# Performance work log

Hardware: AMD Instinct MI355X
Metric: run time of the kernel (lower is better)

Reference implementation:

```python
import jax, jax.numpy as jnp
import numpy as np


def setup_inputs() -> dict:
    key = jax.random.key(0)
    k1, k2 = jax.random.split(key)
    surfaces = jax.random.normal(k1, (4, 4096, 3), dtype=jnp.float32)   # [S, N, K]
    targets = jax.random.normal(k2, (16384, 3), dtype=jnp.float32)      # [M, K]
    return {"surfaces": surfaces, "targets": targets}


def reference(surfaces, targets):
    # Pairwise squared distances ||a-b||^2 = ||a||^2 + ||b||^2 - 2 a.b
    # surfaces: [S, N, K], targets: [M, K]
    a2 = jnp.sum(surfaces * surfaces, axis=-1)          # [S, N]
    b2 = jnp.sum(targets * targets, axis=-1)            # [M]
    ab = jnp.einsum('snk,mk->snm', surfaces, targets)   # [S, N, M]
    dist = a2[:, :, None] + b2[None, None, :] - 2.0 * ab  # [S, N, M]
    # direction='cloud2nearest' -> dim=0: min over surface points N per target
    nearest = jnp.min(dist, axis=1)                     # [S, M]
    # stack over surfaces then min over dim 0 (S)
    nearest = jnp.min(nearest, axis=0)                  # [M]
    return jnp.sum(nearest)
```

## Files before the change

### kernel.cpp

```cpp
#include <hip/hip_runtime.h>
#include <cfloat>


namespace {
constexpr int M   = 16384;
constexpr int SN  = 16384;
constexpr int TPB = 256;
constexpr int T   = 8;
constexpr int TGT_PER_BLOCK = TPB * T;
constexpr int NCHUNK = 128;
constexpr int CHUNK  = SN / NCHUNK;
constexpr int K2B    = 256;
}

__global__ __launch_bounds__(TPB, 4) void dist_partial_min(
    const float* __restrict__ surf,
    const float* __restrict__ tgt,
    float* __restrict__ wmin,
    unsigned* __restrict__ counter)
{
  __shared__ alignas(16) float4 spt[CHUNK];

  const int tid   = threadIdx.x;
  const int mbase = blockIdx.x * TGT_PER_BLOCK;
  const int cbase = blockIdx.y * CHUNK;

  if (blockIdx.x == 0 && blockIdx.y == 0 && tid == 0) counter[0] = 0u;

  if (tid < CHUNK) {
    const float* s = surf + (size_t)(cbase + tid) * 3;
    const float x = s[0], y = s[1], z = s[2];
    spt[tid] = make_float4(x, y, z, fmaf(x, x, fmaf(y, y, z * z)));
  }

  float tx[T], ty[T], tz[T], b2[T], mn[T];
#pragma unroll
  for (int j = 0; j < T; ++j) {
    const int m     = mbase + j * TPB + tid;
    const float* tp = tgt + (size_t)m * 3;
    const float a = tp[0], b = tp[1], c = tp[2];
    tx[j] = -2.0f * a; ty[j] = -2.0f * b; tz[j] = -2.0f * c;
    b2[j] = fmaf(a, a, fmaf(b, b, c * c));
    mn[j] = FLT_MAX;
  }
  __syncthreads();

  float4 C0 = spt[0], C1 = spt[1], C2 = spt[2], C3 = spt[3];
  for (int p = 0; p < CHUNK; p += 4) {
    const int pn = (p + 4) & (CHUNK - 1);
    const float4 N0 = spt[pn + 0];
    const float4 N1 = spt[pn + 1];
    const float4 N2 = spt[pn + 2];
    const float4 N3 = spt[pn + 3];
#pragma unroll
    for (int j = 0; j < T; ++j) {
      const float d0 = fmaf(C0.x, tx[j], fmaf(C0.y, ty[j], fmaf(C0.z, tz[j], C0.w)));
      const float d1 = fmaf(C1.x, tx[j], fmaf(C1.y, ty[j], fmaf(C1.z, tz[j], C1.w)));
      const float d2 = fmaf(C2.x, tx[j], fmaf(C2.y, ty[j], fmaf(C2.z, tz[j], C2.w)));
      const float d3 = fmaf(C3.x, tx[j], fmaf(C3.y, ty[j], fmaf(C3.z, tz[j], C3.w)));
      mn[j] = fminf(fminf(mn[j], d0), d1);
      mn[j] = fminf(fminf(mn[j], d2), d3);
    }
    C0 = N0; C1 = N1; C2 = N2; C3 = N3;
  }

#pragma unroll
  for (int j = 0; j < T; ++j)
    wmin[(size_t)blockIdx.y * M + mbase + j * TPB + tid] = mn[j] + b2[j];
}

__global__ __launch_bounds__(256) void dist_min_sum(
    const float* __restrict__ wmin,
    float* __restrict__ part,
    unsigned* __restrict__ counter,
    float* __restrict__ out)
{
  const int tid  = threadIdx.x;
  const int lane = tid & 63;
  const int w    = tid >> 6;
  const int m    = blockIdx.x * 64 + lane;

  float mnv = FLT_MAX;
  const int c0 = w * (NCHUNK / 4);
#pragma unroll 8
  for (int c = 0; c < NCHUNK / 4; ++c)
    mnv = fminf(mnv, wmin[(size_t)(c0 + c) * M + m]);

  __shared__ float red[4][64];
  red[w][lane] = mnv;
  __syncthreads();

  if (w == 0) {
    float v = fminf(fminf(red[0][lane], red[1][lane]),
                    fminf(red[2][lane], red[3][lane]));
    for (int off = 32; off; off >>= 1) v += __shfl_down(v, off, 64);

    unsigned done = 0;
    if (lane == 0) {
      part[blockIdx.x] = v;
      __threadfence();
      done = atomicAdd(counter, 1u);
    }
    done = __shfl(done, 0, 64);

    if (done == (unsigned)(K2B - 1)) {
      __threadfence();
      float s = 0.0f;
#pragma unroll
      for (int i = 0; i < K2B / 64; ++i) s += part[i * 64 + lane];
      for (int off = 32; off; off >>= 1) s += __shfl_down(s, off, 64);
      if (lane == 0) out[0] = s;
    }
  }
}

extern "C" void kernel_launch(void* const* d_in, const int* in_sizes, int n_in,
                              void* d_out, int out_size, void* d_ws, size_t ws_size,
                              hipStream_t stream) {
  const float* surf = (const float*)d_in[0];
  const float* tgt  = (const float*)d_in[1];
  float* out = (float*)d_out;

  float*    wmin    = (float*)d_ws;
  float*    part    = wmin + (size_t)NCHUNK * M;
  unsigned* counter = (unsigned*)(part + K2B);

  dim3 g1(M / TGT_PER_BLOCK, NCHUNK);
  dist_partial_min<<<g1, TPB, 0, stream>>>(surf, tgt, wmin, counter);
  dist_min_sum<<<K2B, 256, 0, stream>>>(wmin, part, counter, out);
}
```

Measured before the change: 40.34 us.

## Compute pairwise distances with bf16 split-precision MFMA instead of scalar FMA

Adds a prep kernel that encodes surface points and targets as hi/lo bf16 split rows, padded to K=32, so that one 16x16x32 MFMA produces a² − 2a·b with roughly fp32 accuracy. The main kernel streams surface rows from global memory into the matrix cores and reduces each output tile with fminf. It uses 32 chunks instead of 128, which shrinks the partial-min buffer, and b² is now added in the final reduction. This trades VALU FMA work for matrix-core throughput at the cost of an extra launch, zero-padded K, and some loss of precision from the bf16 splitting.

```diff
diff --git a/kernel.cpp b/kernel.cpp
--- a/kernel.cpp
+++ b/kernel.cpp
@@ -5,72 +5,133 @@
 namespace {
 constexpr int M   = 16384;
 constexpr int SN  = 16384;
-constexpr int TPB = 256;
-constexpr int T   = 8;
-constexpr int TGT_PER_BLOCK = TPB * T;
-constexpr int NCHUNK = 128;
-constexpr int CHUNK  = SN / NCHUNK;
-constexpr int K2B    = 256;
+constexpr int NCH = 32;
+constexpr int PPC = SN / NCH;
+constexpr int NG  = 128;
+constexpr int TPG = 128;
+constexpr int K2B = 256;
 }
 
-__global__ __launch_bounds__(TPB, 4) void dist_partial_min(
-    const float* __restrict__ surf,
-    const float* __restrict__ tgt,
-    float* __restrict__ wmin,
-    unsigned* __restrict__ counter)
+typedef short bf16x8 __attribute__((ext_vector_type(8)));
+typedef float f32x4  __attribute__((ext_vector_type(4)));
+
+static __device__ __forceinline__ unsigned short f2bf(float f) {
+  unsigned int u = __builtin_bit_cast(unsigned int, f);
+  return (unsigned short)((u + 0x7FFFu + ((u >> 16) & 1u)) >> 16);
+}
+static __device__ __forceinline__ float bf2f(unsigned short h) {
+  unsigned int u = ((unsigned int)h) << 16;
+  return __builtin_bit_cast(float, u);
+}
+
+__global__ __launch_bounds__(256) void build_ab(
+    const float* __restrict__ surf, const float* __restrict__ tgt,
+    unsigned short* __restrict__ Aex, unsigned short* __restrict__ Bex,
+    float* __restrict__ b2f, unsigned* __restrict__ counter)
 {
-  __shared__ alignas(16) float4 spt[CHUNK];
+  const int i = blockIdx.x * 256 + threadIdx.x;
+  if (i == 0) counter[0] = 0u;
 
-  const int tid   = threadIdx.x;
-  const int mbase = blockIdx.x * TGT_PER_BLOCK;
-  const int cbase = blockIdx.y * CHUNK;
+  {
+    const float x = surf[(size_t)i*3+0], y = surf[(size_t)i*3+1], z = surf[(size_t)i*3+2];
+    const float s2 = fmaf(x, x, fmaf(y, y, z * z));
+    unsigned short row[32];
+#pragma unroll
+    for (int k = 0; k < 32; ++k) row[k] = 0;
+    const float cs[3] = {x, y, z};
+#pragma unroll
+    for (int c = 0; c < 3; ++c) {
+      const unsigned short hi = f2bf(cs[c]);
+      const unsigned short lo = f2bf(cs[c] - bf2f(hi));
+      row[3*c+0] = hi; row[3*c+1] = hi; row[3*c+2] = lo;
+    }
+    const unsigned short shi = f2bf(s2);
+    const unsigned short slo = f2bf(s2 - bf2f(shi));
+    row[9] = shi; row[10] = slo;
+#pragma unroll
+    for (int k = 0; k < 16; ++k)
+      ((unsigned int*)(Aex + (size_t)i*32))[k] =
+          (unsigned int)row[2*k] | ((unsigned int)row[2*k+1] << 16);
+  }
+  {
+    const float a = tgt[(size_t)i*3+0], b = tgt[(size_t)i*3+1], c = tgt[(size_t)i*3+2];
+    b2f[i] = fmaf(a, a, fmaf(b, b, c * c));
+    const float us[3] = {-2.0f*a, -2.0f*b, -2.0f*c};
+    unsigned short row[32];
+#pragma unroll
+    for (int k = 0; k < 32; ++k) row[k] = 0;
+#pragma unroll
+    for (int q = 0; q < 3; ++q) {
+      const unsigned short hi = f2bf(us[q]);
+      const unsigned short lo = f2bf(us[q] - bf2f(hi));
+      row[3*q+0] = hi; row[3*q+1] = lo; row[3*q+2] = hi;
+    }
+    const unsigned short one = f2bf(1.0f);
+    row[9] = one; row[10] = one;
+#pragma unroll
+    for (int k = 0; k < 16; ++k)
+      ((unsigned int*)(Bex + (size_t)i*32))[k] =
+          (unsigned int)row[2*k] | ((unsigned int)row[2*k+1] << 16);
+  }
+}
 
-  if (blockIdx.x == 0 && blockIdx.y == 0 && tid == 0) counter[0] = 0u;
+__global__ __launch_bounds__(256, 4) void dist_mfma(
+    const unsigned short* __restrict__ Aex,
+    const unsigned short* __restrict__ Bex,
+    float* __restrict__ wmin)
+{
+  const int tid  = threadIdx.x;
+  const int lane = tid & 63;
+  const int wid  = tid >> 6;
+  const int wg   = blockIdx.x * 4 + wid;
+  const int g    = wg & (NG - 1);
+  const int c    = wg >> 7;
+  const int m0   = g * TPG;
+  const int r15  = lane & 15;
+  const int koff = (lane >> 4) * 8;
 
-  if (tid < CHUNK) {
-    const float* s = surf + (size_t)(cbase + tid) * 3;
-    const float x = s[0], y = s[1], z = s[2];
-    spt[tid] = make_float4(x, y, z, fmaf(x, x, fmaf(y, y, z * z)));
-  }
+  bf16x8 bfr[8];
+#pragma unroll
+  for (int f = 0; f < 8; ++f)
+    bfr[f] = *(const bf16x8*)(Bex + ((size_t)(m0 + f*16 + r15)) * 32 + koff);
 
-  float tx[T], ty[T], tz[T], b2[T], mn[T];
+  float mn[8];
 #pragma unroll
-  for (int j = 0; j < T; ++j) {
-    const int m     = mbase + j * TPB + tid;
-    const float* tp = tgt + (size_t)m * 3;
-    const float a = tp[0], b = tp[1], c = tp[2];
-    tx[j] = -2.0f * a; ty[j] = -2.0f * b; tz[j] = -2.0f * c;
-    b2[j] = fmaf(a, a, fmaf(b, b, c * c));
-    mn[j] = FLT_MAX;
-  }
-  __syncthreads();
+  for (int f = 0; f < 8; ++f) mn[f] = FLT_MAX;
 
-  float4 C0 = spt[0], C1 = spt[1], C2 = spt[2], C3 = spt[3];
-  for (int p = 0; p < CHUNK; p += 4) {
-    const int pn = (p + 4) & (CHUNK - 1);
-    const float4 N0 = spt[pn + 0];
-    const float4 N1 = spt[pn + 1];
-    const float4 N2 = spt[pn + 2];
-    const float4 N3 = spt[pn + 3];
+  const int pbase = c * PPC;
+  const unsigned short* ap = Aex + ((size_t)(pbase + r15)) * 32 + koff;
+
+  bf16x8 acur = *(const bf16x8*)ap;
+  for (int r = 0; r < PPC / 16; ++r) {
+    const int rn = (r + 1 < PPC / 16) ? r + 1 : r;
+    const bf16x8 anxt = *(const bf16x8*)(ap + (size_t)rn * 16 * 32);
 #pragma unroll
-    for (int j = 0; j < T; ++j) {
-      const float d0 = fmaf(C0.x, tx[j], fmaf(C0.y, ty[j], fmaf(C0.z, tz[j], C0.w)));
-      const float d1 = fmaf(C1.x, tx[j], fmaf(C1.y, ty[j], fmaf(C1.z, tz[j], C1.w)));
-      const float d2 = fmaf(C2.x, tx[j], fmaf(C2.y, ty[j], fmaf(C2.z, tz[j], C2.w)));
-      const float d3 = fmaf(C3.x, tx[j], fmaf(C3.y, ty[j], fmaf(C3.z, tz[j], C3.w)));
-      mn[j] = fminf(fminf(mn[j], d0), d1);
-      mn[j] = fminf(fminf(mn[j], d2), d3);
+    for (int f = 0; f < 8; ++f) {
+      const f32x4 d = __builtin_amdgcn_mfma_f32_16x16x32_bf16(
+          acur, bfr[f], (f32x4){0.f, 0.f, 0.f, 0.f}, 0, 0, 0);
+      mn[f] = fminf(fminf(mn[f], fminf(d[0], d[1])), fminf(d[2], d[3]));
     }
-    C0 = N0; C1 = N1; C2 = N2; C3 = N3;
+    acur = anxt;
   }
 
 #pragma unroll
-  for (int j = 0; j < T; ++j)
-    wmin[(size_t)blockIdx.y * M + mbase + j * TPB + tid] = mn[j] + b2[j];
+  for (int f = 0; f < 8; ++f) {
+    float v = mn[f];
+    v = fminf(v, __shfl_xor(v, 16, 64));
+    v = fminf(v, __shfl_xor(v, 32, 64));
+    mn[f] = v;
+  }
+  if (lane < 16) {
+#pragma unroll
+    for (int f = 0; f < 8; ++f)
+      wmin[(size_t)c * M + m0 + f * 16 + lane] = mn[f];
+  }
 }
 
 __global__ __launch_bounds__(256) void dist_min_sum(
     const float* __restrict__ wmin,
+    const float* __restrict__ b2f,
     float* __restrict__ part,
     unsigned* __restrict__ counter,
     float* __restrict__ out)
@@ -81,10 +142,10 @@
   const int m    = blockIdx.x * 64 + lane;
 
   float mnv = FLT_MAX;
-  const int c0 = w * (NCHUNK / 4);
-#pragma unroll 8
-  for (int c = 0; c < NCHUNK / 4; ++c)
-    mnv = fminf(mnv, wmin[(size_t)(c0 + c) * M + m]);
+  const int c0 = w * (NCH / 4);
+#pragma unroll
+  for (int ci = 0; ci < NCH / 4; ++ci)
+    mnv = fminf(mnv, wmin[(size_t)(c0 + ci) * M + m]);
 
   __shared__ float red[4][64];
   red[w][lane] = mnv;
@@ -93,6 +154,7 @@
   if (w == 0) {
     float v = fminf(fminf(red[0][lane], red[1][lane]),
                     fminf(red[2][lane], red[3][lane]));
+    v += b2f[m];
     for (int off = 32; off; off >>= 1) v += __shfl_down(v, off, 64);
 
     unsigned done = 0;
@@ -121,11 +183,14 @@
   const float* tgt  = (const float*)d_in[1];
   float* out = (float*)d_out;
 
-  float*    wmin    = (float*)d_ws;
-  float*    part    = wmin + (size_t)NCHUNK * M;
+  unsigned short* Aex = (unsigned short*)d_ws;
+  unsigned short* Bex = Aex + (size_t)SN * 32;
+  float* b2f  = (float*)(Bex + (size_t)M * 32);
+  float* wmin = b2f + M;
+  float* part = wmin + (size_t)NCH * M;
   unsigned* counter = (unsigned*)(part + K2B);
 
-  dim3 g1(M / TGT_PER_BLOCK, NCHUNK);
-  dist_partial_min<<<g1, TPB, 0, stream>>>(surf, tgt, wmin, counter);
-  dist_min_sum<<<K2B, 256, 0, stream>>>(wmin, part, counter, out);
+  build_ab<<<SN / 256, 256, 0, stream>>>(surf, tgt, Aex, Bex, b2f, counter);
+  dist_mfma<<<(NG * NCH) / 4, 256, 0, stream>>>(Aex, Bex, wmin);
+  dist_min_sum<<<K2B, 256, 0, stream>>>(wmin, b2f, part, counter, out);
 }
```

Result: no change. 40.44 us, median of 2 (+0.3%).
